# Optimization experiments

Measured on AMD Instinct MI355X. Metric: run time of the kernel, lower is better.

The kernel has to match this reference:

```python
import jax, jax.numpy as jnp
import numpy as np

BSZ, SEQLEN, DIM = 2, 2048, 4096
N_HEADS, N_KV_HEADS, HEAD_DIM = 32, 8, 128
N_REP = N_HEADS // N_KV_HEADS
MAX_SEQ_LEN = 2048
ROPE_THETA = 500000.0
NEG_INF = -1e9


def setup_inputs() -> dict:
    key = jax.random.key(0)
    ks = jax.random.split(key, 6)
    scale = 0.02
    x = jax.random.normal(ks[0], (BSZ, SEQLEN, DIM), dtype=jnp.float32)
    wq = jax.random.normal(ks[1], (DIM, N_HEADS * HEAD_DIM), dtype=jnp.float32) * scale
    wk = jax.random.normal(ks[2], (DIM, N_KV_HEADS * HEAD_DIM), dtype=jnp.float32) * scale
    wv = jax.random.normal(ks[3], (DIM, N_KV_HEADS * HEAD_DIM), dtype=jnp.float32) * scale
    wo = jax.random.normal(ks[4], (N_HEADS * HEAD_DIM, DIM), dtype=jnp.float32) * scale
    # RoPE frequencies (llama precompute_freqs_cis)
    inv_freq = 1.0 / (ROPE_THETA ** (jnp.arange(0, HEAD_DIM, 2, dtype=jnp.float32) / HEAD_DIM))
    t = jnp.arange(SEQLEN, dtype=jnp.float32)
    freqs = jnp.outer(t, inv_freq)  # [seqlen, head_dim//2]
    freqs_cos = jnp.cos(freqs)
    freqs_sin = jnp.sin(freqs)
    # causal additive mask for prefill (start_pos=0)
    mask = jnp.triu(jnp.full((SEQLEN, SEQLEN), NEG_INF, dtype=jnp.float32), k=1)
    cache_k = jnp.zeros((BSZ, MAX_SEQ_LEN, N_KV_HEADS, HEAD_DIM), dtype=jnp.float32)
    cache_v = jnp.zeros((BSZ, MAX_SEQ_LEN, N_KV_HEADS, HEAD_DIM), dtype=jnp.float32)
    return {"x": x, "wq": wq, "wk": wk, "wv": wv, "wo": wo,
            "freqs_cos": freqs_cos, "freqs_sin": freqs_sin, "mask": mask,
            "cache_k": cache_k, "cache_v": cache_v, "start_pos": 0}


def apply_rotary_emb(x, cos, sin):
    # x: [b, s, h, d]; cos/sin: [s, d//2]
    x2 = x.reshape(*x.shape[:-1], -1, 2)
    xe, xo = x2[..., 0], x2[..., 1]
    c = cos[None, :, None, :]
    s = sin[None, :, None, :]
    oe = xe * c - xo * s
    oo = xe * s + xo * c
    return jnp.stack([oe, oo], axis=-1).reshape(x.shape)


def repeat_kv(x, n_rep):
    # [b, k, n_kv, d] -> [b, k, n_kv*n_rep, d]
    b, k, h, d = x.shape
    return jnp.broadcast_to(x[:, :, :, None, :], (b, k, h, n_rep, d)).reshape(b, k, h * n_rep, d)


def reference(x, wq, wk, wv, wo, freqs_cos, freqs_sin, mask, cache_k, cache_v, start_pos):
    bsz, seqlen, _ = x.shape
    xq = (x @ wq).reshape(bsz, seqlen, N_HEADS, HEAD_DIM)
    xk = (x @ wk).reshape(bsz, seqlen, N_KV_HEADS, HEAD_DIM)
    xv = (x @ wv).reshape(bsz, seqlen, N_KV_HEADS, HEAD_DIM)
    xq = apply_rotary_emb(xq, freqs_cos, freqs_sin)
    xk = apply_rotary_emb(xk, freqs_cos, freqs_sin)
    # KV-cache append
    cache_k = jax.lax.dynamic_update_slice(cache_k, xk, (0, start_pos, 0, 0))
    cache_v = jax.lax.dynamic_update_slice(cache_v, xv, (0, start_pos, 0, 0))
    kv_len = start_pos + seqlen
    keys = repeat_kv(cache_k[:, :kv_len], N_REP)      # [b, k, H, d]
    values = repeat_kv(cache_v[:, :kv_len], N_REP)
    q = xq.transpose(0, 2, 1, 3)                      # [b, H, s, d]
    k = keys.transpose(0, 2, 1, 3)
    v = values.transpose(0, 2, 1, 3)
    scores = jnp.einsum('bhsd,bhkd->bhsk', q, k) / jnp.sqrt(jnp.float32(HEAD_DIM))
    scores = scores + mask[None, None, :, :]
    probs = jax.nn.softmax(scores.astype(jnp.float32), axis=-1).astype(q.dtype)
    out = jnp.einsum('bhsk,bhkd->bhsd', probs, v)
    out = out.transpose(0, 2, 1, 3).reshape(bsz, seqlen, -1)
    return out @ wo
```

## Files before the change

kernel.cpp:

```cpp
#include <hip/hip_runtime.h>
#include <hip/hip_bf16.h>

typedef __bf16 bf16_t;
typedef __attribute__((ext_vector_type(4))) __bf16 bf16x4;
typedef __attribute__((ext_vector_type(8))) __bf16 bf16x8;
typedef __attribute__((ext_vector_type(4))) float f32x4;

#define DIM   4096
#define NQKV  6144
#define S_LEN 2048
#define HD    128

__device__ __forceinline__ void gload_lds16(const void* g, void* l) {
  __builtin_amdgcn_global_load_lds(
      (__attribute__((address_space(1))) void*)(g),
      (__attribute__((address_space(3))) void*)(l), 16, 0, 0);
}

__global__ __launch_bounds__(256) void convert_bf16(const float* __restrict__ src,
                                                    bf16_t* __restrict__ dst) {
  size_t i = ((size_t)blockIdx.x * 256 + threadIdx.x) * 8;
  f32x4 a = *(const f32x4*)(src + i);
  f32x4 b = *(const f32x4*)(src + i + 4);
  bf16x8 o;
#pragma unroll
  for (int j = 0; j < 4; ++j) { o[j] = (bf16_t)a[j]; o[4 + j] = (bf16_t)b[j]; }
  *(bf16x8*)(dst + i) = o;
}

__global__ __launch_bounds__(256) void transpose_conv(const float* __restrict__ src,
                                                      bf16_t* __restrict__ dst,
                                                      int K, int N) {
  __shared__ float tile[64][65];
  const int k0 = blockIdx.y * 64, n0 = blockIdx.x * 64;
  const int t = threadIdx.x;
#pragma unroll
  for (int p = 0; p < 4; ++p) {
    int idx = p * 256 + t;
    int r = idx >> 4, c4 = (idx & 15) * 4;
    f32x4 v = *(const f32x4*)&src[(size_t)(k0 + r) * N + n0 + c4];
    tile[r][c4] = v[0]; tile[r][c4 + 1] = v[1];
    tile[r][c4 + 2] = v[2]; tile[r][c4 + 3] = v[3];
  }
  __syncthreads();
#pragma unroll
  for (int p = 0; p < 4; ++p) {
    int idx = p * 256 + t;
    int r = idx >> 4, c4 = (idx & 15) * 4;
    bf16x4 o;
    o[0] = (bf16_t)tile[c4][r];     o[1] = (bf16_t)tile[c4 + 1][r];
    o[2] = (bf16_t)tile[c4 + 2][r]; o[3] = (bf16_t)tile[c4 + 3][r];
    *(bf16x4*)&dst[(size_t)(n0 + r) * K + k0 + c4] = o;
  }
}

template <typename CT, bool ROPE>
__global__ __launch_bounds__(512) void gemm256(const bf16_t* __restrict__ A,
                                               const bf16_t* __restrict__ Bt,
                                               CT* __restrict__ C,
                                               int N, int nbx,
                                               const float* __restrict__ cosT,
                                               const float* __restrict__ sinT) {
  __shared__ __align__(16) bf16_t As[32768];
  __shared__ __align__(16) bf16_t Bs[32768];
  const int tid  = threadIdx.x;
  const int lane = tid & 63;
  const int w    = tid >> 6;
  const int wm   = w >> 2, wn = w & 3;
  const int l15 = lane & 15, l4 = lane >> 4, l7 = lane & 7;

  const int cpx = gridDim.x >> 3;
  const int swz = (blockIdx.x & 7) * cpx + (blockIdx.x >> 3);
  const int by = swz / nbx, bx = swz - by * nbx;
  const int bm = by * 256, bn = bx * 256;

  const size_t g_off0 = (size_t)((w * 2 + 0) * 8 + (lane >> 3)) * 4096
                      + (((lane & 7) ^ ((lane >> 3) & 7)) * 8);
  const size_t g_off1 = g_off0 + (size_t)8 * 4096;
  const int l_off0 = (w * 2 + 0) * 512;
  const int l_off1 = (w * 2 + 1) * 512;

#define STAGE(gsrc, ldst) do { \
    gload_lds16((gsrc) + g_off0, (ldst) + l_off0); \
    gload_lds16((gsrc) + g_off1, (ldst) + l_off1); } while (0)

  const bf16_t* Ab = A  + (size_t)bm * 4096;
  const bf16_t* Bb = Bt + (size_t)bn * 4096;
  const size_t HLF = (size_t)128 * 4096;

  f32x4 acc[8][4];
#pragma unroll
  for (int i = 0; i < 8; ++i)
#pragma unroll
    for (int j = 0; j < 4; ++j) { f32x4 z = {0.f, 0.f, 0.f, 0.f}; acc[i][j] = z; }

  STAGE(Bb,             Bs);
  STAGE(Ab,             As);
  STAGE(Bb + HLF,       Bs + 8192);
  STAGE(Ab + HLF,       As + 8192);
  STAGE(Bb + 64,        Bs + 16384);
  STAGE(Ab + 64,        As + 16384);
  STAGE(Bb + HLF + 64,  Bs + 16384 + 8192);
  asm volatile("s_waitcnt vmcnt(6)" ::: "memory");
  __builtin_amdgcn_s_barrier();

  for (int t = 0; t < 64; ++t) {
    const int cu = t & 1;
    bf16_t* Ac = As + cu * 16384;
    bf16_t* Bc = Bs + cu * 16384;
    bf16_t* Axn = As + (cu ^ 1) * 16384;
    const bf16_t* A1g = Ab + (size_t)(t + 1) * 64;
    const bf16_t* A2g = Ab + (size_t)(t + 2) * 64;
    const bf16_t* B2g = Bb + (size_t)(t + 2) * 64;

    bf16x8 af[4][2], b0[2][2], b1[2][2];

#pragma unroll
    for (int f = 0; f < 4; ++f)
#pragma unroll
      for (int kh = 0; kh < 2; ++kh)
        af[f][kh] = *(const bf16x8*)&Ac[(wm * 64 + f * 16 + l15) * 64 + (((kh * 4 + l4) ^ l7) * 8)];
#pragma unroll
    for (int fb = 0; fb < 2; ++fb)
#pragma unroll
      for (int kh = 0; kh < 2; ++kh)
        b0[fb][kh] = *(const bf16x8*)&Bc[(wn * 32 + fb * 16 + l15) * 64 + (((kh * 4 + l4) ^ l7) * 8)];
    if (t + 1 < 64) STAGE(A1g + HLF, Axn + 8192);
    __builtin_amdgcn_s_barrier();
    asm volatile("s_waitcnt lgkmcnt(0)" ::: "memory");
    __builtin_amdgcn_sched_barrier(0);
    __builtin_amdgcn_s_setprio(1);
#pragma unroll
    for (int f = 0; f < 4; ++f)
#pragma unroll
      for (int fb = 0; fb < 2; ++fb)
#pragma unroll
        for (int kh = 0; kh < 2; ++kh)
          acc[f][fb] = __builtin_amdgcn_mfma_f32_16x16x32_bf16(af[f][kh], b0[fb][kh], acc[f][fb], 0, 0, 0);
    __builtin_amdgcn_s_setprio(0);
    __builtin_amdgcn_s_barrier();

#pragma unroll
    for (int fb = 0; fb < 2; ++fb)
#pragma unroll
      for (int kh = 0; kh < 2; ++kh)
        b1[fb][kh] = *(const bf16x8*)&Bc[8192 + (wn * 32 + fb * 16 + l15) * 64 + (((kh * 4 + l4) ^ l7) * 8)];
    if (t + 2 < 64) STAGE(B2g, Bc);
    __builtin_amdgcn_s_barrier();
    asm volatile("s_waitcnt lgkmcnt(0)" ::: "memory");
    __builtin_amdgcn_sched_barrier(0);
    __builtin_amdgcn_s_setprio(1);
#pragma unroll
    for (int f = 0; f < 4; ++f)
#pragma unroll
      for (int fb = 0; fb < 2; ++fb)
#pragma unroll
        for (int kh = 0; kh < 2; ++kh)
          acc[f][2 + fb] = __builtin_amdgcn_mfma_f32_16x16x32_bf16(af[f][kh], b1[fb][kh], acc[f][2 + fb], 0, 0, 0);
    __builtin_amdgcn_s_setprio(0);
    __builtin_amdgcn_s_barrier();

#pragma unroll
    for (int f = 0; f < 4; ++f)
#pragma unroll
      for (int kh = 0; kh < 2; ++kh)
        af[f][kh] = *(const bf16x8*)&Ac[8192 + (wm * 64 + f * 16 + l15) * 64 + (((kh * 4 + l4) ^ l7) * 8)];
    if (t + 2 < 64) STAGE(A2g, Ac);
    __builtin_amdgcn_s_barrier();
    asm volatile("s_waitcnt lgkmcnt(0)" ::: "memory");
    __builtin_amdgcn_sched_barrier(0);
    __builtin_amdgcn_s_setprio(1);
#pragma unroll
    for (int f = 0; f < 4; ++f)
#pragma unroll
      for (int fb = 0; fb < 2; ++fb)
#pragma unroll
        for (int kh = 0; kh < 2; ++kh)
          acc[4 + f][fb] = __builtin_amdgcn_mfma_f32_16x16x32_bf16(af[f][kh], b0[fb][kh], acc[4 + f][fb], 0, 0, 0);
    __builtin_amdgcn_s_setprio(0);
    __builtin_amdgcn_s_barrier();

    if (t + 2 < 64) STAGE(B2g + HLF, Bc + 8192);
    __builtin_amdgcn_s_barrier();
    __builtin_amdgcn_s_setprio(1);
#pragma unroll
    for (int f = 0; f < 4; ++f)
#pragma unroll
      for (int fb = 0; fb < 2; ++fb)
#pragma unroll
        for (int kh = 0; kh < 2; ++kh)
          acc[4 + f][2 + fb] = __builtin_amdgcn_mfma_f32_16x16x32_bf16(af[f][kh], b1[fb][kh], acc[4 + f][2 + fb], 0, 0, 0);
    __builtin_amdgcn_s_setprio(0);
    if (t < 62)       asm volatile("s_waitcnt vmcnt(6)" ::: "memory");
    else if (t == 62) asm volatile("s_waitcnt vmcnt(0)" ::: "memory");
    __builtin_amdgcn_s_barrier();
  }
#undef STAGE

#pragma unroll
  for (int mi = 0; mi < 8; ++mi) {
    int row0 = bm + (mi >> 2) * 128 + wm * 64 + (mi & 3) * 16 + l4 * 4;
#pragma unroll
    for (int ni = 0; ni < 4; ++ni) {
      int col = bn + (ni >> 1) * 128 + wn * 32 + (ni & 1) * 16 + l15;
      if (ROPE && col < 5120) {
        const int i = (col & 127) >> 1;
        const bool isq = (col < 4096);
        const float scl = isq ? 0.12751745f : 1.0f;
#pragma unroll
        for (int r = 0; r < 4; ++r) {
          int srow = (row0 + r) & (S_LEN - 1);
          float c = cosT[srow * 64 + i] * scl;
          float s = sinT[srow * 64 + i] * scl;
          float a = acc[mi][ni][r];
          float p = __shfl_xor(a, 1);
          float o = (l15 & 1) ? (p * s + a * c) : (a * c - p * s);
          C[(size_t)(row0 + r) * N + col] = (CT)o;
        }
      } else {
#pragma unroll
        for (int r = 0; r < 4; ++r)
          C[(size_t)(row0 + r) * N + col] = (CT)acc[mi][ni][r];
      }
    }
  }
}

__global__ __launch_bounds__(256) void attn_fwd(const bf16_t* __restrict__ qkv,
                                                bf16_t* __restrict__ out) {
  const int pr = blockIdx.x;
  const int h  = blockIdx.y;
  const int b  = blockIdx.z;
  const int kvh = h >> 2;
  const int tid = threadIdx.x;
  const int w    = tid >> 6;
  const int lane = tid & 63;
  const int qloc = lane & 15;
  const int g    = lane >> 4;

  __shared__ __align__(16) bf16_t Ks[2][64 * 128];
  __shared__ __align__(16) bf16_t Vt[128 * 64];

  const bf16_t* kvbase = qkv + (size_t)b * S_LEN * NQKV + DIM + kvh * HD;
  const int vrow_t = tid >> 4;
  const int vcol_t = (tid & 15) * 8;

  const float M2 = 11.5415603f;

#pragma unroll 1
  for (int half = 0; half < 2; ++half) {
    const int qt = half ? pr : 15 - pr;
    const int W = qt * 128 + w * 32;
    const int nt = 2 * qt + 2;

    bf16x8 aq[2][4];
#pragma unroll
    for (int qb = 0; qb < 2; ++qb) {
      const bf16_t* qptr = qkv + (size_t)(b * S_LEN + W + qb * 16 + qloc) * NQKV + h * HD + g * 8;
#pragma unroll
      for (int c = 0; c < 4; ++c) aq[qb][c] = *(const bf16x8*)(qptr + c * 32);
    }

    f32x4 oacc[2][8];
    float lsum[2] = {0.f, 0.f};
#pragma unroll
    for (int qb = 0; qb < 2; ++qb)
#pragma unroll
      for (int d = 0; d < 8; ++d) { f32x4 z = {0.f, 0.f, 0.f, 0.f}; oacc[qb][d] = z; }

    bf16x8 vreg[4];
#pragma unroll
    for (int p = 0; p < 4; ++p) {
      int chunk = p * 4 + w;
      int krow = chunk * 4 + g;
      int key = (krow & 3) | (((krow >> 3) & 1) << 2);
      gload_lds16(kvbase + (size_t)krow * NQKV + ((qloc ^ key) * 8), &Ks[0][chunk * 512]);
    }
#pragma unroll
    for (int p = 0; p < 4; ++p)
      vreg[p] = *(const bf16x8*)(kvbase + 1024 + (size_t)(p * 16 + vrow_t) * NQKV + vcol_t);

#pragma unroll 1
    for (int t = 0; t < nt; ++t) {
      const int kv0 = t * 64;
      const int cur = t & 1;

      if (t + 1 < nt) {
        const int kvn = kv0 + 64;
#pragma unroll
        for (int p = 0; p < 4; ++p) {
          int chunk = p * 4 + w;
          int krow = chunk * 4 + g;
          int key = (krow & 3) | (((krow >> 3) & 1) << 2);
          gload_lds16(kvbase + (size_t)(kvn + krow) * NQKV + ((qloc ^ key) * 8),
                      &Ks[cur ^ 1][chunk * 512]);
        }
        asm volatile("s_waitcnt vmcnt(4)" ::: "memory");
      } else {
        asm volatile("s_waitcnt vmcnt(0)" ::: "memory");
      }

#pragma unroll
      for (int p = 0; p < 4; ++p) {
        int vrow = p * 16 + vrow_t;
        int rk = (vrow >> 3) ^ (tid & 7);
#pragma unroll
        for (int j = 0; j < 8; ++j)
          Vt[(vcol_t + j) * 64 + ((rk ^ j) * 8) + (vrow & 7)] = vreg[p][j];
      }
      if (t + 1 < nt) {
        const int kvn = kv0 + 64;
#pragma unroll
        for (int p = 0; p < 4; ++p)
          vreg[p] = *(const bf16x8*)(kvbase + 1024 + (size_t)(kvn + p * 16 + vrow_t) * NQKV + vcol_t);
      }
      asm volatile("s_waitcnt lgkmcnt(0)" ::: "memory");
      __builtin_amdgcn_s_barrier();

      if (kv0 <= W + 31) {
        f32x4 sacc[2][2][2];
#pragma unroll
        for (int qb = 0; qb < 2; ++qb)
#pragma unroll
          for (int w2 = 0; w2 < 2; ++w2)
#pragma unroll
            for (int hf = 0; hf < 2; ++hf) { f32x4 z = {0.f, 0.f, 0.f, 0.f}; sacc[qb][w2][hf] = z; }
#pragma unroll
        for (int w2 = 0; w2 < 2; ++w2)
#pragma unroll
          for (int hf = 0; hf < 2; ++hf) {
            int r = 32 * w2 + 8 * (qloc >> 2) + 4 * hf + (qloc & 3);
            int key = (r & 3) | (((r >> 3) & 1) << 2);
            bf16x8 bk[4];
#pragma unroll
            for (int c = 0; c < 4; ++c)
              bk[c] = *(const bf16x8*)&Ks[cur][r * 128 + (((c * 4 + g) ^ key) * 8)];
            __builtin_amdgcn_s_setprio(1);
#pragma unroll
            for (int qb = 0; qb < 2; ++qb)
#pragma unroll
              for (int c = 0; c < 4; ++c)
                sacc[qb][w2][hf] = __builtin_amdgcn_mfma_f32_16x16x32_bf16(bk[c], aq[qb][c], sacc[qb][w2][hf], 0, 0, 0);
            __builtin_amdgcn_s_setprio(0);
          }

        const bool diag = (kv0 + 63 > W);
        bf16x8 pa[2][2];
#pragma unroll
        for (int qb = 0; qb < 2; ++qb) {
          const int qg = W + qb * 16 + qloc;
#pragma unroll
          for (int w2 = 0; w2 < 2; ++w2)
#pragma unroll
            for (int hf = 0; hf < 2; ++hf)
#pragma unroll
              for (int r = 0; r < 4; ++r) {
                float e = exp2f(sacc[qb][w2][hf][r] - M2);
                if (diag) {
                  int kg = kv0 + 32 * w2 + 8 * g + 4 * hf + r;
                  e = (kg <= qg) ? e : 0.f;
                }
                lsum[qb] += e;
                pa[qb][w2][hf * 4 + r] = (bf16_t)e;
              }
        }

#pragma unroll
        for (int w2 = 0; w2 < 2; ++w2)
#pragma unroll
          for (int dt = 0; dt < 8; ++dt) {
            int d = dt * 16 + qloc;
            int key2 = (4 * w2 + g) ^ (d & 7) ^ ((d >> 3) & 7);
            bf16x8 bv = *(const bf16x8*)&Vt[d * 64 + key2 * 8];
            __builtin_amdgcn_s_setprio(1);
#pragma unroll
            for (int qb = 0; qb < 2; ++qb)
              oacc[qb][dt] = __builtin_amdgcn_mfma_f32_16x16x32_bf16(bv, pa[qb][w2], oacc[qb][dt], 0, 0, 0);
            __builtin_amdgcn_s_setprio(0);
          }
      }
      __builtin_amdgcn_s_barrier();
    }

#pragma unroll
    for (int qb = 0; qb < 2; ++qb) {
      float ls = lsum[qb];
      ls += __shfl_xor(ls, 16);
      ls += __shfl_xor(ls, 32);
      float inv = 1.f / ls;
      bf16_t* op = out + (size_t)(b * S_LEN + W + qb * 16 + qloc) * DIM + h * HD;
#pragma unroll
      for (int dt = 0; dt < 8; ++dt) {
        bf16x4 o4;
#pragma unroll
        for (int r = 0; r < 4; ++r) o4[r] = (bf16_t)(oacc[qb][dt][r] * inv);
        *(bf16x4*)(op + dt * 16 + 4 * g) = o4;
      }
    }
  }
}

extern "C" void kernel_launch(void* const* d_in, const int* in_sizes, int n_in,
                              void* d_out, int out_size, void* d_ws, size_t ws_size,
                              hipStream_t stream) {
  const float* x  = (const float*)d_in[0];
  const float* wq = (const float*)d_in[1];
  const float* wk = (const float*)d_in[2];
  const float* wv = (const float*)d_in[3];
  const float* wo = (const float*)d_in[4];
  const float* fc = (const float*)d_in[5];
  const float* fs = (const float*)d_in[6];

  bf16_t* ws    = (bf16_t*)d_ws;
  bf16_t* wqkvT = ws;
  bf16_t* woT   = wqkvT + (size_t)6144 * 4096;
  bf16_t* qkv   = woT   + (size_t)4096 * 4096;
  bf16_t* xb    = qkv   + (size_t)4096 * 6144;
  bf16_t* ao    = xb;

  convert_bf16<<<8192, 256, 0, stream>>>(x, xb);
  transpose_conv<<<dim3(64, 64), 256, 0, stream>>>(wq, wqkvT, 4096, 4096);
  transpose_conv<<<dim3(16, 64), 256, 0, stream>>>(wk, wqkvT + (size_t)4096 * 4096, 4096, 1024);
  transpose_conv<<<dim3(16, 64), 256, 0, stream>>>(wv, wqkvT + (size_t)5120 * 4096, 4096, 1024);
  transpose_conv<<<dim3(64, 64), 256, 0, stream>>>(wo, woT, 4096, 4096);

  gemm256<bf16_t, true><<<384, 512, 0, stream>>>(xb, wqkvT, qkv, 6144, 24, fc, fs);
  attn_fwd<<<dim3(8, 32, 2), 256, 0, stream>>>(qkv, ao);
  gemm256<float, false><<<256, 512, 0, stream>>>(ao, woT, (float*)d_out, 4096, 16, nullptr, nullptr);
}
```

Measured before the change: 607.5 us.

## Double-buffer the transposed V tile to overlap its LDS writes with compute

The transposed V tile in LDS is now double-buffered. The next tile's V registers are scattered into the alternate buffer while the current QK^T, softmax and PV MFMAs run. This cuts each KV iteration to a single barrier, and the next K/V global loads are issued at the top of the iteration, ahead of compute. The cost is a larger LDS footprint per block, which may lower how many blocks fit on a CU at once.

```diff
diff --git a/kernel.cpp b/kernel.cpp
--- a/kernel.cpp
+++ b/kernel.cpp
@@ -239,7 +239,7 @@
   const int g    = lane >> 4;
 
   __shared__ __align__(16) bf16_t Ks[2][64 * 128];
-  __shared__ __align__(16) bf16_t Vt[128 * 64];
+  __shared__ __align__(16) bf16_t Vt[2][128 * 64];
 
   const bf16_t* kvbase = qkv + (size_t)b * S_LEN * NQKV + DIM + kvh * HD;
   const int vrow_t = tid >> 4;
@@ -270,23 +270,38 @@
 
     bf16x8 vreg[4];
 #pragma unroll
+    for (int p = 0; p < 4; ++p)
+      vreg[p] = *(const bf16x8*)(kvbase + 1024 + (size_t)(p * 16 + vrow_t) * NQKV + vcol_t);
+#pragma unroll
     for (int p = 0; p < 4; ++p) {
       int chunk = p * 4 + w;
       int krow = chunk * 4 + g;
       int key = (krow & 3) | (((krow >> 3) & 1) << 2);
       gload_lds16(kvbase + (size_t)krow * NQKV + ((qloc ^ key) * 8), &Ks[0][chunk * 512]);
     }
-#pragma unroll
-    for (int p = 0; p < 4; ++p)
-      vreg[p] = *(const bf16x8*)(kvbase + 1024 + (size_t)(p * 16 + vrow_t) * NQKV + vcol_t);
+    asm volatile("s_waitcnt vmcnt(4)" ::: "memory");
+#pragma unroll
+    for (int p = 0; p < 4; ++p) {
+      int vrow = p * 16 + vrow_t;
+      int rk = (vrow >> 3) ^ (tid & 7);
+#pragma unroll
+      for (int j = 0; j < 8; ++j)
+        Vt[0][(vcol_t + j) * 64 + ((rk ^ j) * 8) + (vrow & 7)] = vreg[p][j];
+    }
+    asm volatile("s_waitcnt vmcnt(0) lgkmcnt(0)" ::: "memory");
+    __builtin_amdgcn_s_barrier();
 
 #pragma unroll 1
     for (int t = 0; t < nt; ++t) {
       const int kv0 = t * 64;
       const int cur = t & 1;
-
-      if (t + 1 < nt) {
+      const bool more = (t + 1 < nt);
+
+      if (more) {
         const int kvn = kv0 + 64;
+#pragma unroll
+        for (int p = 0; p < 4; ++p)
+          vreg[p] = *(const bf16x8*)(kvbase + 1024 + (size_t)(kvn + p * 16 + vrow_t) * NQKV + vcol_t);
 #pragma unroll
         for (int p = 0; p < 4; ++p) {
           int chunk = p * 4 + w;
@@ -295,30 +310,11 @@
           gload_lds16(kvbase + (size_t)(kvn + krow) * NQKV + ((qloc ^ key) * 8),
                       &Ks[cur ^ 1][chunk * 512]);
         }
-        asm volatile("s_waitcnt vmcnt(4)" ::: "memory");
-      } else {
-        asm volatile("s_waitcnt vmcnt(0)" ::: "memory");
-      }
-
-#pragma unroll
-      for (int p = 0; p < 4; ++p) {
-        int vrow = p * 16 + vrow_t;
-        int rk = (vrow >> 3) ^ (tid & 7);
-#pragma unroll
-        for (int j = 0; j < 8; ++j)
-          Vt[(vcol_t + j) * 64 + ((rk ^ j) * 8) + (vrow & 7)] = vreg[p][j];
-      }
-      if (t + 1 < nt) {
-        const int kvn = kv0 + 64;
-#pragma unroll
-        for (int p = 0; p < 4; ++p)
-          vreg[p] = *(const bf16x8*)(kvbase + 1024 + (size_t)(kvn + p * 16 + vrow_t) * NQKV + vcol_t);
-      }
-      asm volatile("s_waitcnt lgkmcnt(0)" ::: "memory");
-      __builtin_amdgcn_s_barrier();
-
-      if (kv0 <= W + 31) {
-        f32x4 sacc[2][2][2];
+      }
+
+      const bool compute = (kv0 <= W + 31);
+      f32x4 sacc[2][2][2];
+      if (compute) {
 #pragma unroll
         for (int qb = 0; qb < 2; ++qb)
 #pragma unroll
@@ -343,9 +339,13 @@
                 sacc[qb][w2][hf] = __builtin_amdgcn_mfma_f32_16x16x32_bf16(bk[c], aq[qb][c], sacc[qb][w2][hf], 0, 0, 0);
             __builtin_amdgcn_s_setprio(0);
           }
-
+      }
+
+      if (more) asm volatile("s_waitcnt vmcnt(4)" ::: "memory");
+
+      bf16x8 pa[2][2];
+      if (compute) {
         const bool diag = (kv0 + 63 > W);
-        bf16x8 pa[2][2];
 #pragma unroll
         for (int qb = 0; qb < 2; ++qb) {
           const int qg = W + qb * 16 + qloc;
@@ -364,14 +364,27 @@
                 pa[qb][w2][hf * 4 + r] = (bf16_t)e;
               }
         }
-
+      }
+
+      if (more) {
+#pragma unroll
+        for (int p = 0; p < 4; ++p) {
+          int vrow = p * 16 + vrow_t;
+          int rk = (vrow >> 3) ^ (tid & 7);
+#pragma unroll
+          for (int j = 0; j < 8; ++j)
+            Vt[cur ^ 1][(vcol_t + j) * 64 + ((rk ^ j) * 8) + (vrow & 7)] = vreg[p][j];
+        }
+      }
+
+      if (compute) {
 #pragma unroll
         for (int w2 = 0; w2 < 2; ++w2)
 #pragma unroll
           for (int dt = 0; dt < 8; ++dt) {
             int d = dt * 16 + qloc;
             int key2 = (4 * w2 + g) ^ (d & 7) ^ ((d >> 3) & 7);
-            bf16x8 bv = *(const bf16x8*)&Vt[d * 64 + key2 * 8];
+            bf16x8 bv = *(const bf16x8*)&Vt[cur][d * 64 + key2 * 8];
             __builtin_amdgcn_s_setprio(1);
 #pragma unroll
             for (int qb = 0; qb < 2; ++qb)
@@ -379,6 +392,8 @@
             __builtin_amdgcn_s_setprio(0);
           }
       }
+
+      asm volatile("s_waitcnt vmcnt(0) lgkmcnt(0)" ::: "memory");
       __builtin_amdgcn_s_barrier();
     }
 
```

New measurement: 628.6 us. 1.03x slower.
